# Kernel tuning notes

Measured on AMD Instinct MI355X. Metric: run time of the kernel, lower is better.

Reference implementation:

```python
import jax, jax.numpy as jnp
import numpy as np

MAX_BRANCHES = 4
MAX_DEPTH = 3
BEAM_WIDTH = 2
TEMPERATURE = 0.8
MIN_SCORE_DIFF = 0.1


def _gelu(x):
    return jax.nn.gelu(x, approximate=False)  # torch nn.GELU default is exact erf


def _evaluate(x, We1, be1, We2, be2, We3, be3):
    # evaluator: Linear(H,2H) -> GELU -> Linear(2H,H) -> GELU -> Linear(H,1) -> Sigmoid
    h = _gelu(x @ We1 + be1)
    h = _gelu(h @ We2 + be2)
    return jax.nn.sigmoid(h @ We3 + be3)[..., 0]


def setup_inputs() -> dict:
    key = jax.random.key(0)
    B, S, H = 8, 2048, 512
    ks = jax.random.split(key, 8)
    s1 = 1.0 / np.sqrt(H)
    s2 = 1.0 / np.sqrt(2 * H)
    f32 = jnp.float32
    return {
        "hidden_states": jax.random.normal(ks[0], (B, S, H), f32),
        "We1": (jax.random.normal(ks[1], (H, 2 * H), f32) * s1),
        "be1": jnp.zeros((2 * H,), f32),
        "We2": (jax.random.normal(ks[2], (2 * H, H), f32) * s2),
        "be2": jnp.zeros((H,), f32),
        "We3": (jax.random.normal(ks[3], (H, 1), f32) * s1),
        "be3": jnp.zeros((1,), f32),
        "Wp": (jax.random.normal(ks[4], (H, H), f32) * s1),
        "bp": jnp.zeros((H,), f32),
        "Wb": (jax.random.normal(ks[5], (MAX_BRANCHES, H, H), f32) * s1),
        "bb": jnp.zeros((MAX_BRANCHES, H), f32),
    }


def reference(hidden_states, We1, be1, We2, be2, We3, be3, Wp, bp, Wb, bb):
    B, S, H = hidden_states.shape
    ev = lambda x: _evaluate(x, We1, be1, We2, be2, We3, be3)

    x0 = jnp.swapaxes(hidden_states, 0, 1)        # [S, B, H] positions independent
    beam_states = x0[:, None]                     # [S, K=1, B, H]
    beam_scores = ev(x0).mean(-1)[:, None]        # [S, 1] root score (mean over batch)

    for _ in range(MAX_DEPTH):
        K = beam_states.shape[1]
        proj = beam_states @ Wp + bp                                  # [S,K,B,H]
        # fixed per-branch projection + GELU -> thoughts [S,K,N,B,H]
        th = _gelu(jnp.einsum('skbh,nhj->sknbj', proj, Wb)
                   + bb[None, None, :, None, :])
        sc = ev(th).mean(-1) / TEMPERATURE                            # [S,K,N]

        # min_score_diff dedup: keep branch i iff no previously-kept score within
        # MIN_SCORE_DIFF and fewer than BEAM_WIDTH kept so far (static loop over 4)
        keep = jnp.zeros(sc.shape, bool)
        count = jnp.zeros(sc.shape[:-1], sc.dtype)
        for i in range(MAX_BRANCHES):
            mind = jnp.where(keep, jnp.abs(sc[..., i:i + 1] - sc), jnp.inf).min(-1)
            ki = ((count == 0) | (mind >= MIN_SCORE_DIFF)) & (count < BEAM_WIDTH)
            keep = keep.at[..., i].set(ki)
            count = count + ki.astype(count.dtype)

        cand_sc = jnp.where(keep, sc, -jnp.inf).reshape(S, K * MAX_BRANCHES)
        cand_st = th.reshape(S, K * MAX_BRANCHES, B, H)
        top_sc, top_idx = jax.lax.top_k(cand_sc, BEAM_WIDTH)          # sorted desc
        top_st = jnp.take_along_axis(cand_st, top_idx[:, :, None, None], axis=1)
        # fewer than BEAM_WIDTH survivors -> duplicate the best (same final result)
        valid = jnp.isfinite(top_sc)
        beam_scores = jnp.where(valid, top_sc, top_sc[:, :1])
        beam_states = jnp.where(valid[:, :, None, None], top_st, top_st[:, :1])

    best = beam_states[:, 0]                      # beam sorted desc -> slot 0 is best leaf
    return jnp.swapaxes(best, 0, 1) + hidden_states
```

## Files before the change

### kernel.cpp

```cpp
#include <hip/hip_runtime.h>

#define S_  2048
#define B_  8
#define H_  512
#define H2_ 1024
#define CM_ 8192

typedef _Float16 f16x8 __attribute__((ext_vector_type(8)));
typedef _Float16 f16x4 __attribute__((ext_vector_type(4)));
typedef float    f32x4 __attribute__((ext_vector_type(4)));

__device__ __forceinline__ float gelu_f(float x){
    return 0.5f * x * (1.0f + erff(x * 0.7071067811865476f));
}

__global__ __launch_bounds__(256)
void prep_k(const float* __restrict__ src, _Float16* __restrict__ dst,
            int K, int N)
{
    int g = blockIdx.x * 256 + threadIdx.x;
    int KS = K >> 5;
    int l  = g & 63;
    int rem = g >> 6;
    int ks = rem % KS;
    int fc = rem / KS;
    int kbase = ks * 32 + (l >> 4) * 8;
    int col   = fc * 16 + (l & 15);
    size_t KN = (size_t)K * N;
    #pragma unroll
    for (int j = 0; j < 8; j++) {
        float x = src[(size_t)(kbase + j) * N + col];
        _Float16 h1 = (_Float16)x;
        float r = x - (float)h1;
        _Float16 h2 = (_Float16)(r * 2048.0f);
        dst[(size_t)g * 8 + j]      = h1;
        dst[KN + (size_t)g * 8 + j] = h2;
    }
}

template<bool GELU, int INMAP, int OUTMAP>
__global__ __launch_bounds__(256, 2)
void mgemm_k(const float* __restrict__ A, const _Float16* __restrict__ Bp,
             const float* __restrict__ bias, float* __restrict__ C,
             int N, int K, int r0, const int* __restrict__ sel, int nsel)
{
    __shared__ __align__(16) char smem[8192];
    const int t    = threadIdx.x;
    const int m0   = blockIdx.x * 64;
    const int n0   = blockIdx.y * 128;
    const int lane = t & 63;
    const int wave = t >> 6;
    const int wr   = wave >> 1;
    const int wc   = wave & 1;
    const int KS   = K >> 5;
    const size_t planeStride = (size_t)K * N;

    const int srow = t >> 3;
    const int sk0  = (t & 7) * 4;
    const float* aptr[2];
    int wbyte[2];
    #pragma unroll
    for (int q = 0; q < 2; q++) {
        int row = srow + 32 * q;
        int r = m0 + row;
        size_t aoff;
        if (INMAP == 1) { int gr = r0 + r; aoff = ((size_t)(gr & 7) * S_ + (gr >> 3)) * H_; }
        else if (INMAP == 2) {
            int s = r >> 4, j = (r >> 3) & 1, b = r & 7;
            int kb = sel[s * 2 + j] >> 2;
            aoff = ((size_t)(s * 2 + kb) * 8 + b) * H_;
        }
        else if (INMAP == 3) { int s = r >> 4, b = r & 7; aoff = ((size_t)b * S_ + s) * H_; }
        else aoff = (size_t)r * K;
        aptr[q] = A + aoff + sk0;
        int e = (row & 15) + 16 * (sk0 >> 3);
        int p = e ^ (((e >> 4) & 3) << 2);
        wbyte[q] = (row >> 4) * 1024 + p * 16 + (sk0 & 4) * 2;
    }

    const int rl    = lane ^ (((lane >> 4) & 3) << 2);
    const int rbyte = rl * 16;

    const _Float16* bjp[4];
    #pragma unroll
    for (int j = 0; j < 4; j++) {
        int fcg = (n0 >> 4) + wc * 4 + j;
        bjp[j] = Bp + (size_t)fcg * KS * 512 + lane * 8;
    }

    f32x4 accM[2][4], accX[2][4];
    #pragma unroll
    for (int i = 0; i < 2; i++)
        #pragma unroll
        for (int j = 0; j < 4; j++) { accM[i][j] = (f32x4)0.0f; accX[i][j] = (f32x4)0.0f; }

    for (int ks = 0; ks < KS; ks++) {
        float4 av[2];
        #pragma unroll
        for (int q = 0; q < 2; q++) av[q] = *(const float4*)(aptr[q] + ks * 32);
        f16x8 b1v[4], b2v[4];
        #pragma unroll
        for (int j = 0; j < 4; j++) {
            const _Float16* bp = bjp[j] + (size_t)ks * 512;
            b1v[j] = *(const f16x8*)(bp);
            b2v[j] = *(const f16x8*)(bp + planeStride);
        }

        __syncthreads();
        #pragma unroll
        for (int q = 0; q < 2; q++) {
            const float xs[4] = {av[q].x, av[q].y, av[q].z, av[q].w};
            f16x4 hv1, hv2;
            #pragma unroll
            for (int e = 0; e < 4; e++) {
                float x = xs[e];
                _Float16 h1 = (_Float16)x;
                hv1[e] = h1;
                hv2[e] = (_Float16)((x - (float)h1) * 2048.0f);
            }
            *(f16x4*)(smem + wbyte[q])        = hv1;
            *(f16x4*)(smem + 4096 + wbyte[q]) = hv2;
        }
        __syncthreads();

        f16x8 a1[2], a2[2];
        #pragma unroll
        for (int i = 0; i < 2; i++) {
            int off = (wr * 2 + i) * 1024 + rbyte;
            a1[i] = *(const f16x8*)(smem + off);
            a2[i] = *(const f16x8*)(smem + 4096 + off);
        }
        #pragma unroll
        for (int i = 0; i < 2; i++)
            #pragma unroll
            for (int j = 0; j < 4; j++)
                accM[i][j] = __builtin_amdgcn_mfma_f32_16x16x32_f16(a1[i], b1v[j], accM[i][j], 0, 0, 0);
        #pragma unroll
        for (int i = 0; i < 2; i++)
            #pragma unroll
            for (int j = 0; j < 4; j++)
                accX[i][j] = __builtin_amdgcn_mfma_f32_16x16x32_f16(a1[i], b2v[j], accX[i][j], 0, 0, 0);
        #pragma unroll
        for (int i = 0; i < 2; i++)
            #pragma unroll
            for (int j = 0; j < 4; j++)
                accX[i][j] = __builtin_amdgcn_mfma_f32_16x16x32_f16(a2[i], b1v[j], accX[i][j], 0, 0, 0);
    }

    const float inv2048 = 4.8828125e-4f;
    #pragma unroll
    for (int i = 0; i < 2; i++) {
        int rbase = m0 + wr * 32 + i * 16 + ((lane >> 4) << 2);
        bool ok = true;
        if (OUTMAP == 1) ok = ((sel[rbase >> 3] & 3) == nsel);
        if (!ok) continue;
        #pragma unroll
        for (int j = 0; j < 4; j++) {
            int col = n0 + wc * 64 + j * 16 + (lane & 15);
            float bv = bias[col];
            #pragma unroll
            for (int r = 0; r < 4; r++) {
                float c = accM[i][j][r] + accX[i][j][r] * inv2048 + bv;
                if (GELU) c = gelu_f(c);
                C[(size_t)(rbase + r) * N + col] = c;
            }
        }
    }
}

__global__ __launch_bounds__(256)
void score1_k(const float* __restrict__ h2, const float* __restrict__ We3,
              const float* __restrict__ be3, float* __restrict__ ev,
              int pr0, int n)
{
    int row  = blockIdx.x * 4 + (threadIdx.x >> 6);
    int lane = threadIdx.x & 63;
    const float* p = h2 + (size_t)row * H_;
    float s = 0.f;
    #pragma unroll
    for (int j = 0; j < H_ / 64; j++) s += p[lane + 64 * j] * We3[lane + 64 * j];
    #pragma unroll
    for (int off = 32; off > 0; off >>= 1) s += __shfl_down(s, off, 64);
    if (lane == 0) {
        int pr = pr0 + row;
        ev[(size_t)(pr >> 3) * 32 + n * 8 + (pr & 7)] = 1.0f / (1.0f + expf(-(s + be3[0])));
    }
}

__global__ __launch_bounds__(256)
void score2_k(const float* __restrict__ ev, float* __restrict__ sc, int n)
{
    int i = blockIdx.x * 256 + threadIdx.x;
    if (i >= n) return;
    float s = 0.f;
    #pragma unroll
    for (int b = 0; b < 8; b++) s += ev[i * 8 + b];
    sc[i] = (s * 0.125f) / 0.8f;
}

__global__ __launch_bounds__(256)
void select_k(const float* __restrict__ sc, int* __restrict__ sel, int K)
{
    int s = blockIdx.x * 256 + threadIdx.x;
    if (s >= S_) return;
    int K4 = K * 4;
    float cand[8];
    for (int k = 0; k < K; k++) {
        const float* scp = sc + (size_t)(s * K + k) * 4;
        bool keep[4] = {false, false, false, false};
        int count = 0;
        for (int i = 0; i < 4; i++) {
            float mind = INFINITY;
            for (int j = 0; j < 4; j++)
                if (keep[j]) mind = fminf(mind, fabsf(scp[i] - scp[j]));
            bool ki = ((count == 0) || (mind >= 0.1f)) && (count < 2);
            keep[i] = ki;
            if (ki) count++;
        }
        for (int i = 0; i < 4; i++) cand[k * 4 + i] = keep[i] ? scp[i] : -INFINITY;
    }
    int i0 = 0;
    for (int i = 1; i < K4; i++) if (cand[i] > cand[i0]) i0 = i;
    int i1 = -1;
    for (int i = 0; i < K4; i++) {
        if (i == i0) continue;
        if (i1 < 0 || cand[i] > cand[i1]) i1 = i;
    }
    if (!(cand[i1] > -INFINITY)) i1 = i0;
    sel[s * 2 + 0] = i0;
    sel[s * 2 + 1] = i1;
}

__global__ __launch_bounds__(256)
void final_add_k(const float* __restrict__ beams, const float* __restrict__ hidden,
                 float* __restrict__ out)
{
    size_t tid = (size_t)blockIdx.x * 256 + threadIdx.x;
    const size_t total = (size_t)B_ * S_ * (H_ / 4);
    if (tid >= total) return;
    int h4 = tid & (H_ / 4 - 1);
    int s  = (tid >> 7) & (S_ - 1);
    int b  = tid >> 18;
    float4 v  = ((const float4*)(beams + ((size_t)(s * 2 + 0) * 8 + b) * H_))[h4];
    float4 hd = ((const float4*)(hidden + ((size_t)b * S_ + s) * H_))[h4];
    v.x += hd.x; v.y += hd.y; v.z += hd.z; v.w += hd.w;
    ((float4*)(out + ((size_t)b * S_ + s) * H_))[h4] = v;
}

extern "C" void kernel_launch(void* const* d_in, const int* in_sizes, int n_in,
                              void* d_out, int out_size, void* d_ws, size_t ws_size,
                              hipStream_t stream)
{
    const float* hidden = (const float*)d_in[0];
    const float* We1 = (const float*)d_in[1];
    const float* be1 = (const float*)d_in[2];
    const float* We2 = (const float*)d_in[3];
    const float* be2 = (const float*)d_in[4];
    const float* We3 = (const float*)d_in[5];
    const float* be3 = (const float*)d_in[6];
    const float* Wp  = (const float*)d_in[7];
    const float* bp  = (const float*)d_in[8];
    const float* Wb  = (const float*)d_in[9];
    const float* bb  = (const float*)d_in[10];
    (void)in_sizes; (void)n_in; (void)ws_size;

    float* beams = (float*)d_ws;
    float* R1    = beams + 16777216;
    float* projc = R1;
    float* thc   = R1 + 4194304;
    float* h1    = R1 + 8388608;
    float* h2    = thc;
    float* projg = R1;

    float* outf = (float*)d_out;
    float* wreg = outf + (out_size - 2359296);
    _Float16* WpP  = (_Float16*)wreg;
    _Float16* WbP  = WpP + 524288;
    _Float16* We1P = WbP + 2097152;
    _Float16* We2P = We1P + 1048576;
    float* evb = wreg - 131072;
    float* scb = evb - 16384;
    int*   sel = (int*)(scb - 4096);

    prep_k<<<128, 256, 0, stream>>>(Wp, WpP, 512, 512);
    for (int n = 0; n < 4; n++)
        prep_k<<<128, 256, 0, stream>>>(Wb + (size_t)n * 262144, WbP + (size_t)n * 524288, 512, 512);
    prep_k<<<256, 256, 0, stream>>>(We1, We1P, 512, 1024);
    prep_k<<<256, 256, 0, stream>>>(We2, We2P, 1024, 512);

    for (int d = 0; d < 3; d++) {
        const int K  = (d == 0) ? 1 : 2;
        const int Mp = S_ * K * B_;
        const int NC = Mp / CM_;

        for (int c = 0; c < NC; c++) {
            dim3 gp(CM_ / 64, 4);
            if (d == 0)
                mgemm_k<false, 1, 0><<<gp, 256, 0, stream>>>(hidden, WpP, bp, projc,
                                                             512, 512, c * CM_, nullptr, 0);
            else
                mgemm_k<false, 0, 0><<<gp, 256, 0, stream>>>(beams + (size_t)c * CM_ * H_,
                                                             WpP, bp, projc, 512, 512, 0, nullptr, 0);
            for (int n = 0; n < 4; n++) {
                mgemm_k<true, 0, 0><<<gp, 256, 0, stream>>>(projc, WbP + (size_t)n * 524288,
                                                            bb + n * H_, thc, 512, 512, 0, nullptr, 0);
                dim3 g1(CM_ / 64, 8);
                mgemm_k<true, 0, 0><<<g1, 256, 0, stream>>>(thc, We1P, be1, h1, 1024, 512, 0, nullptr, 0);
                dim3 g2(CM_ / 64, 4);
                mgemm_k<true, 0, 0><<<g2, 256, 0, stream>>>(h1, We2P, be2, h2, 512, 1024, 0, nullptr, 0);
                score1_k<<<CM_ / 4, 256, 0, stream>>>(h2, We3, be3, evb, c * CM_, n);
            }
        }

        const int nsc = S_ * K * 4;
        score2_k<<<(nsc + 255) / 256, 256, 0, stream>>>(evb, scb, nsc);
        select_k<<<(S_ + 255) / 256, 256, 0, stream>>>(scb, sel, K);

        dim3 gg(32768 / 64, 4);
        if (d == 0)
            mgemm_k<false, 3, 0><<<gg, 256, 0, stream>>>(hidden, WpP, bp, projg,
                                                         512, 512, 0, sel, 0);
        else
            mgemm_k<false, 2, 0><<<gg, 256, 0, stream>>>(beams, WpP, bp, projg,
                                                         512, 512, 0, sel, 0);
        for (int n = 0; n < 4; n++)
            mgemm_k<true, 0, 1><<<gg, 256, 0, stream>>>(projg, WbP + (size_t)n * 524288,
                                                        bb + n * H_, beams, 512, 512, 0, sel, n);
    }

    final_add_k<<<(int)(((size_t)B_ * S_ * (H_ / 4) + 255) / 256), 256, 0, stream>>>(
        beams, hidden, outf);
}
```

Measured before the change: 5.186 ms.

## Keep activations in pre-split fp16 MFMA fragment layout across GEMM chain

Intermediate activations (proj, thoughts, h1, beams) are now stored as hi/lo fp16 split planes in MFMA fragment order. The GEMM loads A fragments straight from global memory, with no fp32 load, on-the-fly splitting, LDS staging or per-k-step barriers. The epilogue splits results through shared memory into the fragment layout. The 1024-wide evaluator hidden layer is processed in two 512 halves, with the second half accumulating into an fp32 buffer, which shrinks the workspace. Risks include uncoalesced fragment-order stores, extra epilogue LDS traffic, and more kernel launches from the halved h1 path.

```diff
diff --git a/kernel.cpp b/kernel.cpp
--- a/kernel.cpp
+++ b/kernel.cpp
@@ -2,17 +2,16 @@
 
 #define S_  2048
 #define B_  8
-#define H_  512
-#define H2_ 1024
 #define CM_ 8192
+#define KS_ 16
 
 typedef _Float16 f16x8 __attribute__((ext_vector_type(8)));
-typedef _Float16 f16x4 __attribute__((ext_vector_type(4)));
 typedef float    f32x4 __attribute__((ext_vector_type(4)));
 
 __device__ __forceinline__ float gelu_f(float x){
     return 0.5f * x * (1.0f + erff(x * 0.7071067811865476f));
 }
+
 
 __global__ __launch_bounds__(256)
 void prep_k(const float* __restrict__ src, _Float16* __restrict__ dst,
@@ -31,20 +30,44 @@
     for (int j = 0; j < 8; j++) {
         float x = src[(size_t)(kbase + j) * N + col];
         _Float16 h1 = (_Float16)x;
-        float r = x - (float)h1;
-        _Float16 h2 = (_Float16)(r * 2048.0f);
+        _Float16 h2 = (_Float16)((x - (float)h1) * 2048.0f);
         dst[(size_t)g * 8 + j]      = h1;
         dst[KN + (size_t)g * 8 + j] = h2;
     }
 }
 
-template<bool GELU, int INMAP, int OUTMAP>
-__global__ __launch_bounds__(256, 2)
-void mgemm_k(const float* __restrict__ A, const _Float16* __restrict__ Bp,
-             const float* __restrict__ bias, float* __restrict__ C,
-             int N, int K, int r0, const int* __restrict__ sel, int nsel)
-{
-    __shared__ __align__(16) char smem[8192];
+__global__ __launch_bounds__(256)
+void prep_hidden_k(const float* __restrict__ hidden, _Float16* __restrict__ dst,
+                   size_t PS)
+{
+    int g = blockIdx.x * 256 + threadIdx.x;
+    int l  = g & 63;
+    int rem = g >> 6;
+    int ks = rem & 15;
+    int fr = rem >> 4;
+    int gr = fr * 16 + (l & 15);
+    int s = gr >> 3, b = gr & 7;
+    int kbase = ks * 32 + (l >> 4) * 8;
+    const float* src = hidden + ((size_t)b * S_ + s) * 512 + kbase;
+    #pragma unroll
+    for (int j = 0; j < 8; j++) {
+        float x = src[j];
+        _Float16 h1 = (_Float16)x;
+        _Float16 h2 = (_Float16)((x - (float)h1) * 2048.0f);
+        dst[(size_t)g * 8 + j]      = h1;
+        dst[PS + (size_t)g * 8 + j] = h2;
+    }
+}
+
+template<bool GELU, int EPI, int AMAP, bool PRED>
+__global__ __launch_bounds__(256)
+void fgemm(const _Float16* __restrict__ Ap, size_t aPS,
+           const _Float16* __restrict__ Bp, size_t bPS, int fc0,
+           const float* __restrict__ bias,
+           _Float16* __restrict__ Cp, size_t cPS,
+           float* __restrict__ Cf,
+           const int* __restrict__ sel, int nsel, int r0)
+{
     const int t    = threadIdx.x;
     const int m0   = blockIdx.x * 64;
     const int n0   = blockIdx.y * 128;
@@ -52,40 +75,32 @@
     const int wave = t >> 6;
     const int wr   = wave >> 1;
     const int wc   = wave & 1;
-    const int KS   = K >> 5;
-    const size_t planeStride = (size_t)K * N;
-
-    const int srow = t >> 3;
-    const int sk0  = (t & 7) * 4;
-    const float* aptr[2];
-    int wbyte[2];
-    #pragma unroll
-    for (int q = 0; q < 2; q++) {
-        int row = srow + 32 * q;
-        int r = m0 + row;
-        size_t aoff;
-        if (INMAP == 1) { int gr = r0 + r; aoff = ((size_t)(gr & 7) * S_ + (gr >> 3)) * H_; }
-        else if (INMAP == 2) {
-            int s = r >> 4, j = (r >> 3) & 1, b = r & 7;
+
+    const _Float16* ap[2];
+    #pragma unroll
+    for (int i = 0; i < 2; i++) {
+        if (AMAP == 0) {
+            int tl = (m0 >> 4) + wr * 2 + i;
+            ap[i] = Ap + ((size_t)tl * KS_) * 512 + lane * 8;
+        } else if (AMAP == 2) {
+            int s = ((r0 + m0) >> 4) + wr * 2 + i;
+            int j = (lane >> 3) & 1;
             int kb = sel[s * 2 + j] >> 2;
-            aoff = ((size_t)(s * 2 + kb) * 8 + b) * H_;
-        }
-        else if (INMAP == 3) { int s = r >> 4, b = r & 7; aoff = ((size_t)b * S_ + s) * H_; }
-        else aoff = (size_t)r * K;
-        aptr[q] = A + aoff + sk0;
-        int e = (row & 15) + 16 * (sk0 >> 3);
-        int p = e ^ (((e >> 4) & 3) << 2);
-        wbyte[q] = (row >> 4) * 1024 + p * 16 + (sk0 & 4) * 2;
-    }
-
-    const int rl    = lane ^ (((lane >> 4) & 3) << 2);
-    const int rbyte = rl * 16;
+            int al = (lane & 48) | (kb << 3) | (lane & 7);
+            ap[i] = Ap + ((size_t)s * KS_) * 512 + al * 8;
+        } else {
+            int s = ((r0 + m0) >> 4) + wr * 2 + i;
+            int ti = s >> 1;
+            int al = (lane & 48) | ((s & 1) << 3) | (lane & 7);
+            ap[i] = Ap + ((size_t)ti * KS_) * 512 + al * 8;
+        }
+    }
 
     const _Float16* bjp[4];
     #pragma unroll
     for (int j = 0; j < 4; j++) {
-        int fcg = (n0 >> 4) + wc * 4 + j;
-        bjp[j] = Bp + (size_t)fcg * KS * 512 + lane * 8;
+        int fcg = fc0 + (n0 >> 4) + wc * 4 + j;
+        bjp[j] = Bp + (size_t)fcg * KS_ * 512 + lane * 8;
     }
 
     f32x4 accM[2][4], accX[2][4];
@@ -94,76 +109,96 @@
         #pragma unroll
         for (int j = 0; j < 4; j++) { accM[i][j] = (f32x4)0.0f; accX[i][j] = (f32x4)0.0f; }
 
-    for (int ks = 0; ks < KS; ks++) {
-        float4 av[2];
-        #pragma unroll
-        for (int q = 0; q < 2; q++) av[q] = *(const float4*)(aptr[q] + ks * 32);
-        f16x8 b1v[4], b2v[4];
+    #pragma unroll 2
+    for (int ks = 0; ks < KS_; ks++) {
+        f16x8 a1[2], a2[2], b1[4], b2[4];
+        #pragma unroll
+        for (int i = 0; i < 2; i++) {
+            a1[i] = *(const f16x8*)(ap[i] + (size_t)ks * 512);
+            a2[i] = *(const f16x8*)(ap[i] + aPS + (size_t)ks * 512);
+        }
         #pragma unroll
         for (int j = 0; j < 4; j++) {
-            const _Float16* bp = bjp[j] + (size_t)ks * 512;
-            b1v[j] = *(const f16x8*)(bp);
-            b2v[j] = *(const f16x8*)(bp + planeStride);
-        }
-
-        __syncthreads();
-        #pragma unroll
-        for (int q = 0; q < 2; q++) {
-            const float xs[4] = {av[q].x, av[q].y, av[q].z, av[q].w};
-            f16x4 hv1, hv2;
-            #pragma unroll
-            for (int e = 0; e < 4; e++) {
-                float x = xs[e];
-                _Float16 h1 = (_Float16)x;
-                hv1[e] = h1;
-                hv2[e] = (_Float16)((x - (float)h1) * 2048.0f);
+            b1[j] = *(const f16x8*)(bjp[j] + (size_t)ks * 512);
+            b2[j] = *(const f16x8*)(bjp[j] + bPS + (size_t)ks * 512);
+        }
+        #pragma unroll
+        for (int i = 0; i < 2; i++)
+            #pragma unroll
+            for (int j = 0; j < 4; j++)
+                accM[i][j] = __builtin_amdgcn_mfma_f32_16x16x32_f16(a1[i], b1[j], accM[i][j], 0, 0, 0);
+        #pragma unroll
+        for (int i = 0; i < 2; i++)
+            #pragma unroll
+            for (int j = 0; j < 4; j++)
+                accX[i][j] = __builtin_amdgcn_mfma_f32_16x16x32_f16(a1[i], b2[j], accX[i][j], 0, 0, 0);
+        #pragma unroll
+        for (int i = 0; i < 2; i++)
+            #pragma unroll
+            for (int j = 0; j < 4; j++)
+                accX[i][j] = __builtin_amdgcn_mfma_f32_16x16x32_f16(a2[i], b1[j], accX[i][j], 0, 0, 0);
+    }
+
+    const float inv2048 = 4.8828125e-4f;
+
+    if (EPI == 2 || EPI == 3) {
+        #pragma unroll
+        for (int j = 0; j < 4; j++) {
+            int lc = wc * 64 + j * 16 + (lane & 15);
+            #pragma unroll
+            for (int i = 0; i < 2; i++) {
+                int lr = wr * 32 + i * 16 + ((lane >> 4) << 2);
+                #pragma unroll
+                for (int r = 0; r < 4; r++) {
+                    float c = accM[i][j][r] + accX[i][j][r] * inv2048;
+                    size_t idx = (size_t)(m0 + lr + r) * 512 + n0 + lc;
+                    if (EPI == 3) {
+                        c += Cf[idx] + bias[n0 + lc];
+                        if (GELU) c = gelu_f(c);
+                    }
+                    Cf[idx] = c;
+                }
             }
-            *(f16x4*)(smem + wbyte[q])        = hv1;
-            *(f16x4*)(smem + 4096 + wbyte[q]) = hv2;
-        }
-        __syncthreads();
-
-        f16x8 a1[2], a2[2];
+        }
+        return;
+    }
+
+    __shared__ _Float16 sH1[64][136];
+    __shared__ _Float16 sH2[64][136];
+    #pragma unroll
+    for (int j = 0; j < 4; j++) {
+        int lc = wc * 64 + j * 16 + (lane & 15);
+        float bv = bias[n0 + lc];
         #pragma unroll
         for (int i = 0; i < 2; i++) {
-            int off = (wr * 2 + i) * 1024 + rbyte;
-            a1[i] = *(const f16x8*)(smem + off);
-            a2[i] = *(const f16x8*)(smem + 4096 + off);
-        }
-        #pragma unroll
-        for (int i = 0; i < 2; i++)
-            #pragma unroll
-            for (int j = 0; j < 4; j++)
-                accM[i][j] = __builtin_amdgcn_mfma_f32_16x16x32_f16(a1[i], b1v[j], accM[i][j], 0, 0, 0);
-        #pragma unroll
-        for (int i = 0; i < 2; i++)
-            #pragma unroll
-            for (int j = 0; j < 4; j++)
-                accX[i][j] = __builtin_amdgcn_mfma_f32_16x16x32_f16(a1[i], b2v[j], accX[i][j], 0, 0, 0);
-        #pragma unroll
-        for (int i = 0; i < 2; i++)
-            #pragma unroll
-            for (int j = 0; j < 4; j++)
-                accX[i][j] = __builtin_amdgcn_mfma_f32_16x16x32_f16(a2[i], b1v[j], accX[i][j], 0, 0, 0);
-    }
-
-    const float inv2048 = 4.8828125e-4f;
-    #pragma unroll
-    for (int i = 0; i < 2; i++) {
-        int rbase = m0 + wr * 32 + i * 16 + ((lane >> 4) << 2);
-        bool ok = true;
-        if (OUTMAP == 1) ok = ((sel[rbase >> 3] & 3) == nsel);
-        if (!ok) continue;
-        #pragma unroll
-        for (int j = 0; j < 4; j++) {
-            int col = n0 + wc * 64 + j * 16 + (lane & 15);
-            float bv = bias[col];
+            int lr = wr * 32 + i * 16 + ((lane >> 4) << 2);
             #pragma unroll
             for (int r = 0; r < 4; r++) {
                 float c = accM[i][j][r] + accX[i][j][r] * inv2048 + bv;
                 if (GELU) c = gelu_f(c);
-                C[(size_t)(rbase + r) * N + col] = c;
+                _Float16 h1 = (_Float16)c;
+                sH1[lr + r][lc] = h1;
+                sH2[lr + r][lc] = (_Float16)((c - (float)h1) * 2048.0f);
             }
+        }
+    }
+    __syncthreads();
+
+    bool ok = true;
+    if (PRED) {
+        int prow = r0 + m0 + wave * 16 + (lane & 15);
+        ok = ((sel[prow >> 3] & 3) == nsel);
+    }
+    if (ok) {
+        int row = wave * 16 + (lane & 15);
+        #pragma unroll
+        for (int ksx = 0; ksx < 4; ksx++) {
+            int coff = ksx * 32 + ((lane >> 4) << 3);
+            f16x8 h1v = *(const f16x8*)&sH1[row][coff];
+            f16x8 h2v = *(const f16x8*)&sH2[row][coff];
+            size_t o = (((size_t)((m0 >> 4) + wave) * KS_) + (n0 >> 5) + ksx) * 512 + lane * 8;
+            *(f16x8*)(Cp + o)       = h1v;
+            *(f16x8*)(Cp + cPS + o) = h2v;
         }
     }
 }
@@ -175,10 +210,10 @@
 {
     int row  = blockIdx.x * 4 + (threadIdx.x >> 6);
     int lane = threadIdx.x & 63;
-    const float* p = h2 + (size_t)row * H_;
+    const float* p = h2 + (size_t)row * 512;
     float s = 0.f;
     #pragma unroll
-    for (int j = 0; j < H_ / 64; j++) s += p[lane + 64 * j] * We3[lane + 64 * j];
+    for (int j = 0; j < 8; j++) s += p[lane + 64 * j] * We3[lane + 64 * j];
     #pragma unroll
     for (int off = 32; off > 0; off >>= 1) s += __shfl_down(s, off, 64);
     if (lane == 0) {
@@ -232,19 +267,22 @@
 }
 
 __global__ __launch_bounds__(256)
-void final_add_k(const float* __restrict__ beams, const float* __restrict__ hidden,
-                 float* __restrict__ out)
-{
-    size_t tid = (size_t)blockIdx.x * 256 + threadIdx.x;
-    const size_t total = (size_t)B_ * S_ * (H_ / 4);
-    if (tid >= total) return;
-    int h4 = tid & (H_ / 4 - 1);
-    int s  = (tid >> 7) & (S_ - 1);
-    int b  = tid >> 18;
-    float4 v  = ((const float4*)(beams + ((size_t)(s * 2 + 0) * 8 + b) * H_))[h4];
-    float4 hd = ((const float4*)(hidden + ((size_t)b * S_ + s) * H_))[h4];
-    v.x += hd.x; v.y += hd.y; v.z += hd.z; v.w += hd.w;
-    ((float4*)(out + ((size_t)b * S_ + s) * H_))[h4] = v;
+void final_add_k(const _Float16* __restrict__ beamsF, size_t PS,
+                 const float* __restrict__ hidden, float* __restrict__ out)
+{
+    int tid = blockIdx.x * 256 + threadIdx.x;
+    int oc = tid & 63;
+    int rem = tid >> 6;
+    int b = rem & 7;
+    int s = rem >> 3;
+    size_t o = (((size_t)s * KS_) + (oc >> 2)) * 512 + ((((oc & 3) << 4) | b) * 8);
+    f16x8 m = *(const f16x8*)(beamsF + o);
+    f16x8 x = *(const f16x8*)(beamsF + PS + o);
+    const float* hp = hidden + ((size_t)b * S_ + s) * 512 + oc * 8;
+    float* op = out + ((size_t)b * S_ + s) * 512 + oc * 8;
+    #pragma unroll
+    for (int j = 0; j < 8; j++)
+        op[j] = (float)m[j] + (float)x[j] * 4.8828125e-4f + hp[j];
 }
 
 extern "C" void kernel_launch(void* const* d_in, const int* in_sizes, int n_in,
@@ -264,70 +302,83 @@
     const float* bb  = (const float*)d_in[10];
     (void)in_sizes; (void)n_in; (void)ws_size;
 
-    float* beams = (float*)d_ws;
-    float* R1    = beams + 16777216;
-    float* projc = R1;
-    float* thc   = R1 + 4194304;
-    float* h1    = R1 + 8388608;
-    float* h2    = thc;
-    float* projg = R1;
+    _Float16* beamsF = (_Float16*)d_ws;
+    const size_t PS_B = 16777216;
+    _Float16* R1     = beamsF + 2 * PS_B;
+    const size_t PS_C = 4194304;
+    _Float16* projcF = R1;
+    _Float16* thcF   = R1 + 2 * PS_C;
+    _Float16* h1hF   = R1 + 4 * PS_C;
+    const size_t PS_G = 8388608;
+    _Float16* projgF = R1;
 
     float* outf = (float*)d_out;
-    float* wreg = outf + (out_size - 2359296);
-    _Float16* WpP  = (_Float16*)wreg;
+    float* evb  = outf + (out_size - 131072);
+    float* scb  = evb - 16384;
+    int*   sel  = (int*)(scb - 4096);
+    float* h2f  = (float*)sel - 4194304;
+    _Float16* WpP  = (_Float16*)(h2f - 2359296);
     _Float16* WbP  = WpP + 524288;
     _Float16* We1P = WbP + 2097152;
-    _Float16* We2P = We1P + 1048576;
-    float* evb = wreg - 131072;
-    float* scb = evb - 16384;
-    int*   sel = (int*)(scb - 4096);
+    _Float16* We2Pa= We1P + 1048576;
+    _Float16* We2Pb= We2Pa + 524288;
 
     prep_k<<<128, 256, 0, stream>>>(Wp, WpP, 512, 512);
     for (int n = 0; n < 4; n++)
         prep_k<<<128, 256, 0, stream>>>(Wb + (size_t)n * 262144, WbP + (size_t)n * 524288, 512, 512);
     prep_k<<<256, 256, 0, stream>>>(We1, We1P, 512, 1024);
-    prep_k<<<256, 256, 0, stream>>>(We2, We2P, 1024, 512);
+    prep_k<<<128, 256, 0, stream>>>(We2, We2Pa, 512, 512);
+    prep_k<<<128, 256, 0, stream>>>(We2 + 262144, We2Pb, 512, 512);
+    prep_hidden_k<<<4096, 256, 0, stream>>>(hidden, beamsF, PS_B);
+
+    dim3 g1(128, 4), g2(256, 4);
 
     for (int d = 0; d < 3; d++) {
         const int K  = (d == 0) ? 1 : 2;
-        const int Mp = S_ * K * B_;
-        const int NC = Mp / CM_;
+        const int NC = (d == 0) ? 2 : 4;
 
         for (int c = 0; c < NC; c++) {
-            dim3 gp(CM_ / 64, 4);
-            if (d == 0)
-                mgemm_k<false, 1, 0><<<gp, 256, 0, stream>>>(hidden, WpP, bp, projc,
-                                                             512, 512, c * CM_, nullptr, 0);
-            else
-                mgemm_k<false, 0, 0><<<gp, 256, 0, stream>>>(beams + (size_t)c * CM_ * H_,
-                                                             WpP, bp, projc, 512, 512, 0, nullptr, 0);
+            size_t off = (size_t)c * CM_ * 512;
+            fgemm<false, 0, 0, false><<<g1, 256, 0, stream>>>(
+                beamsF + off, PS_B, WpP, 262144, 0, bp, projcF, PS_C, nullptr, nullptr, 0, 0);
             for (int n = 0; n < 4; n++) {
-                mgemm_k<true, 0, 0><<<gp, 256, 0, stream>>>(projc, WbP + (size_t)n * 524288,
-                                                            bb + n * H_, thc, 512, 512, 0, nullptr, 0);
-                dim3 g1(CM_ / 64, 8);
-                mgemm_k<true, 0, 0><<<g1, 256, 0, stream>>>(thc, We1P, be1, h1, 1024, 512, 0, nullptr, 0);
-                dim3 g2(CM_ / 64, 4);
-                mgemm_k<true, 0, 0><<<g2, 256, 0, stream>>>(h1, We2P, be2, h2, 512, 1024, 0, nullptr, 0);
-                score1_k<<<CM_ / 4, 256, 0, stream>>>(h2, We3, be3, evb, c * CM_, n);
+                fgemm<true, 0, 0, false><<<g1, 256, 0, stream>>>(
+                    projcF, PS_C, WbP + (size_t)n * 524288, 262144, 0, bb + n * 512,
+                    thcF, PS_C, nullptr, nullptr, 0, 0);
+                for (int h = 0; h < 2; h++) {
+                    fgemm<true, 0, 0, false><<<g1, 256, 0, stream>>>(
+                        thcF, PS_C, We1P, 524288, h * 32, be1 + h * 512,
+                        h1hF, PS_C, nullptr, nullptr, 0, 0);
+                    if (h == 0)
+                        fgemm<false, 2, 0, false><<<g1, 256, 0, stream>>>(
+                            h1hF, PS_C, We2Pa, 262144, 0, nullptr, nullptr, 0, h2f, nullptr, 0, 0);
+                    else
+                        fgemm<true, 3, 0, false><<<g1, 256, 0, stream>>>(
+                            h1hF, PS_C, We2Pb, 262144, 0, be2, nullptr, 0, h2f, nullptr, 0, 0);
+                }
+                score1_k<<<2048, 256, 0, stream>>>(h2f, We3, be3, evb, c * CM_, n);
             }
         }
 
         const int nsc = S_ * K * 4;
         score2_k<<<(nsc + 255) / 256, 256, 0, stream>>>(evb, scb, nsc);
-        select_k<<<(S_ + 255) / 256, 256, 0, stream>>>(scb, sel, K);
-
-        dim3 gg(32768 / 64, 4);
-        if (d == 0)
-            mgemm_k<false, 3, 0><<<gg, 256, 0, stream>>>(hidden, WpP, bp, projg,
-                                                         512, 512, 0, sel, 0);
-        else
-            mgemm_k<false, 2, 0><<<gg, 256, 0, stream>>>(beams, WpP, bp, projg,
-                                                         512, 512, 0, sel, 0);
-        for (int n = 0; n < 4; n++)
-            mgemm_k<true, 0, 1><<<gg, 256, 0, stream>>>(projg, WbP + (size_t)n * 524288,
-                                                        bb + n * H_, beams, 512, 512, 0, sel, n);
-    }
-
-    final_add_k<<<(int)(((size_t)B_ * S_ * (H_ / 4) + 255) / 256), 256, 0, stream>>>(
-        beams, hidden, outf);
-}
+        select_k<<<8, 256, 0, stream>>>(scb, sel, K);
+
+        for (int cc = 0; cc < 2; cc++) {
+            int c2 = 1 - cc;
+            int r0 = c2 * 16384;
+            if (d == 0)
+                fgemm<false, 0, 3, false><<<g2, 256, 0, stream>>>(
+                    beamsF, PS_B, WpP, 262144, 0, bp, projgF, PS_G, nullptr, sel, 0, r0);
+            else
+                fgemm<false, 0, 2, false><<<g2, 256, 0, stream>>>(
+                    beamsF, PS_B, WpP, 262144, 0, bp, projgF, PS_G, nullptr, sel, 0, r0);
+            for (int n = 0; n < 4; n++)
+                fgemm<true, 0, 0, true><<<g2, 256, 0, stream>>>(
+                    projgF, PS_G, WbP + (size_t)n * 524288, 262144, 0, bb + n * 512,
+                    beamsF + (size_t)r0 * 512, PS_B, nullptr, sel, n, r0);
+        }
+    }
+
+    final_add_k<<<4096, 256, 0, stream>>>(beamsF, PS_B, hidden, outf);
+}
```

Result: slower. 6.377 ms (+23.0%).
